# Performance work log

Measured on AMD Instinct MI355X. Metric: run time of the kernel, lower is better.

The kernel has to match this reference:

```python
import jax, jax.numpy as jnp
import numpy as np

N_NODES = 50000
N_EDGES = 1600000
IN_DIM = 128
N_HEADS = 8
OUT_DIM = 16
LEAKY_SLOPE = 0.2


def setup_inputs() -> dict:
    key = jax.random.key(0)
    k1, k2, k3, k4, k5, k6 = jax.random.split(key, 6)
    x = jax.random.normal(k1, (N_NODES, IN_DIM), dtype=jnp.float32)
    W = jax.random.normal(k2, (N_HEADS * OUT_DIM, IN_DIM), dtype=jnp.float32) * (1.414 / np.sqrt(IN_DIM))
    attn_l = jax.random.normal(k3, (N_HEADS, OUT_DIM), dtype=jnp.float32) * 0.5
    attn_r = jax.random.normal(k4, (N_HEADS, OUT_DIM), dtype=jnp.float32) * 0.5
    src = jax.random.randint(k5, (N_EDGES,), 0, N_NODES, dtype=jnp.int64) if jax.config.jax_enable_x64 else jax.random.randint(k5, (N_EDGES,), 0, N_NODES, dtype=jnp.int32)
    dst = jax.random.randint(k6, (N_EDGES,), 0, N_NODES, dtype=src.dtype)
    return {"x": x, "W": W, "attn_l": attn_l, "attn_r": attn_r, "src": src, "dst": dst}


def reference(x, W, attn_l, attn_r, src, dst):
    n = x.shape[0]
    # fc projection -> [N, H, D]
    ft = (x @ W.T).reshape(n, N_HEADS, OUT_DIM)
    # per-node attention logits (bmm with [H,D,1] vector == contraction over D) -> [N, H]
    a1 = jnp.einsum('nhd,hd->nh', ft, attn_l)
    a2 = jnp.einsum('nhd,hd->nh', ft, attn_r)
    # per-edge score: leaky_relu(a1[src] + a2[dst]) -> [E, H]
    e = jax.nn.leaky_relu(a1[src] + a2[dst], negative_slope=LEAKY_SLOPE)
    # segment softmax over incoming edges of each dst node (numerically stable)
    seg_max = jax.ops.segment_max(e, dst, num_segments=n)          # [N, H]
    seg_max = jnp.where(jnp.isfinite(seg_max), seg_max, 0.0)       # isolated nodes -> 0
    e_exp = jnp.exp(e - seg_max[dst])                              # [E, H]
    denom = jax.ops.segment_sum(e_exp, dst, num_segments=n)        # [N, H]
    alpha = e_exp / denom[dst]                                     # [E, H]
    # weighted scatter-sum of src messages -> [N, H, D]
    msgs = ft[src] * alpha[:, :, None]                             # [E, H, D]
    out = jax.ops.segment_sum(msgs, dst, num_segments=n)
    return out
```

## Files before the change

kernel.cpp:

```cpp
#include <hip/hip_runtime.h>
#include <math.h>

#define N_NODES 50000
#define N_EDGES 1600000
#define IN_DIM 128
#define N_HEADS 8
#define OUT_DIM 16
#define HD 128
#define NBUCK 784
#define BCAP 2560
#define CHUNK 4096
#define BIN_BLOCKS ((N_EDGES + CHUNK - 1) / CHUNK)
#define NTILE 3125
#define PBLK ((NTILE + 3) / 4)
#define TROW 132
#define LOG2E 1.4426950408889634f

typedef __attribute__((ext_vector_type(8))) short bf16x8;
typedef __attribute__((ext_vector_type(4))) float f32x4;

__device__ __forceinline__ unsigned short f2bf(float f) {
    union { float f; unsigned int u; } v; v.f = f;
    unsigned int u = v.u;
    unsigned int r = (u + 0x7fffu + ((u >> 16) & 1u)) >> 16;
    return (unsigned short)r;
}

__device__ __forceinline__ void scan_nbuck_excl(int* arr, int* part) {
    int t = threadIdx.x;
    int v0 = 0, v1 = 0, v2 = 0, v3 = 0, cs = 0;
    if (t < NBUCK / 4) {
        v0 = arr[4 * t]; v1 = arr[4 * t + 1]; v2 = arr[4 * t + 2]; v3 = arr[4 * t + 3];
        cs = v0 + v1 + v2 + v3;
    }
    part[t] = cs;
    __syncthreads();
    for (int d = 1; d < 256; d <<= 1) {
        int u = (t >= d) ? part[t - d] : 0;
        __syncthreads();
        part[t] += u;
        __syncthreads();
    }
    if (t < NBUCK / 4) {
        int run = part[t] - cs;
        arr[4 * t] = run; run += v0;
        arr[4 * t + 1] = run; run += v1;
        arr[4 * t + 2] = run; run += v2;
        arr[4 * t + 3] = run;
    }
    __syncthreads();
}

__global__ void k_prep(const float* __restrict__ W, unsigned short* __restrict__ Wb,
                       int* __restrict__ bucket_cnt, int* __restrict__ ovf_cnt) {
    int g = blockIdx.x * 256 + threadIdx.x;
    if (g < NBUCK) bucket_cnt[g] = 0;
    if (g == 0) *ovf_cnt = 0;
    if (g >= (HD * IN_DIM) / 4) return;
    float4 v = ((const float4*)W)[g];
    ushort4 us;
    us.x = f2bf(v.x); us.y = f2bf(v.y); us.z = f2bf(v.z); us.w = f2bf(v.w);
    ((ushort4*)Wb)[g] = us;
}

__global__ __launch_bounds__(256) void k_proj_bin(
    const float* __restrict__ x, const unsigned short* __restrict__ Wb,
    const float* __restrict__ attn_l, const float* __restrict__ attn_r,
    unsigned short* __restrict__ ftb, float* __restrict__ a1, float* __restrict__ a2,
    const int* __restrict__ src, const int* __restrict__ dst,
    unsigned int* __restrict__ region, int* __restrict__ bucket_cnt,
    int* __restrict__ ovf_cnt, unsigned int* __restrict__ ovf) {
    __shared__ __align__(16) char smem[4 * 16 * TROW * 4];
    int tid = threadIdx.x;

    if (blockIdx.x < PBLK) {
        int wid  = tid >> 6;
        int tile = blockIdx.x * 4 + wid;
        if (tile >= NTILE) return;
        int lane = tid & 63;
        int m = lane & 15, q = lane >> 4;
        int node0 = tile * 16;

        const float* xr = x + (size_t)(node0 + m) * IN_DIM + q * 8;
        float4 xa[4][2];
#pragma unroll
        for (int ks = 0; ks < 4; ks++) {
            xa[ks][0] = *(const float4*)(xr + ks * 32);
            xa[ks][1] = *(const float4*)(xr + ks * 32 + 4);
        }
        bf16x8 afr[4];
#pragma unroll
        for (int ks = 0; ks < 4; ks++) {
            afr[ks][0] = (short)f2bf(xa[ks][0].x); afr[ks][1] = (short)f2bf(xa[ks][0].y);
            afr[ks][2] = (short)f2bf(xa[ks][0].z); afr[ks][3] = (short)f2bf(xa[ks][0].w);
            afr[ks][4] = (short)f2bf(xa[ks][1].x); afr[ks][5] = (short)f2bf(xa[ks][1].y);
            afr[ks][6] = (short)f2bf(xa[ks][1].z); afr[ks][7] = (short)f2bf(xa[ks][1].w);
        }

        float* tl = (float*)smem + wid * (16 * TROW);

#pragma unroll
        for (int h = 0; h < N_HEADS; h++) {
            const unsigned short* wrow = Wb + (size_t)(h * 16 + m) * IN_DIM + q * 8;
            f32x4 c = {0.f, 0.f, 0.f, 0.f};
#pragma unroll
            for (int ks = 0; ks < 4; ks++) {
                bf16x8 bfr = *(const bf16x8*)(wrow + ks * 32);
                c = __builtin_amdgcn_mfma_f32_16x16x32_bf16(afr[ks], bfr, c, 0, 0, 0);
            }
#pragma unroll
            for (int r = 0; r < 4; r++)
                tl[(q * 4 + r) * TROW + h * 16 + m] = c[r];
        }

        int nd = lane & 15;
#pragma unroll
        for (int hi = 0; hi < 2; hi++) {
            int hh = (lane >> 4) + hi * 4;
            const float4* rowv = (const float4*)(tl + nd * TROW + hh * 16);
            const float4* alv  = (const float4*)(attn_l + hh * OUT_DIM);
            const float4* arv  = (const float4*)(attn_r + hh * OUT_DIM);
            float sl = 0.f, sr = 0.f;
#pragma unroll
            for (int d4 = 0; d4 < 4; d4++) {
                float4 fv = rowv[d4];
                float4 al = alv[d4];
                float4 ar = arv[d4];
                sl += fv.x * al.x + fv.y * al.y + fv.z * al.z + fv.w * al.w;
                sr += fv.x * ar.x + fv.y * ar.y + fv.z * ar.z + fv.w * ar.w;
            }
            a1[(node0 + nd) * N_HEADS + hh] = sl * LOG2E;
            a2[(node0 + nd) * N_HEADS + hh] = sr * LOG2E;
        }

#pragma unroll
        for (int p = 0; p < 4; p++) {
            int r = p * 4 + q;
            const float* srcp = tl + r * TROW + m * 8;
            float4 f0 = *(const float4*)(srcp);
            float4 f1 = *(const float4*)(srcp + 4);
            ushort4 u0, u1;
            u0.x = f2bf(f0.x); u0.y = f2bf(f0.y); u0.z = f2bf(f0.z); u0.w = f2bf(f0.w);
            u1.x = f2bf(f1.x); u1.y = f2bf(f1.y); u1.z = f2bf(f1.z); u1.w = f2bf(f1.w);
            ushort4* dstp = (ushort4*)(ftb + (size_t)(node0 + r) * HD + m * 8);
            dstp[0] = u0;
            dstp[1] = u1;
        }
    } else {
        unsigned int* stage = (unsigned int*)smem;
        int* hist  = (int*)(smem + 16384);
        int* delta = (int*)(smem + 19520);
        int* part  = (int*)(smem + 22656);

        int t = tid;
        int base = (blockIdx.x - PBLK) * CHUNK;
        int nvalid = min(CHUNK, N_EDGES - base);

        for (int i = t; i < NBUCK; i += 256) hist[i] = 0;
        __syncthreads();

        unsigned int mypack[CHUNK / 256];
#pragma unroll
        for (int k = 0; k < CHUNK / 256; k++) {
            int i = t + k * 256;
            if (i < nvalid) {
                int s = src[base + i];
                int d = dst[base + i];
                unsigned int p = ((unsigned int)d << 16) | (unsigned int)s;
                mypack[k] = p;
                atomicAdd(&hist[d >> 6], 1);
            }
        }
        __syncthreads();
        for (int i = t; i < NBUCK; i += 256) {
            int h = hist[i];
            delta[i] = (h > 0) ? atomicAdd(&bucket_cnt[i], h) : 0;
        }
        __syncthreads();
        scan_nbuck_excl(hist, part);
        for (int i = t; i < NBUCK; i += 256) delta[i] -= hist[i];
        __syncthreads();
#pragma unroll
        for (int k = 0; k < CHUNK / 256; k++) {
            int i = t + k * 256;
            if (i < nvalid) {
                unsigned int p = mypack[k];
                int slot = atomicAdd(&hist[p >> 22], 1);
                stage[slot] = p;
            }
        }
        __syncthreads();
        for (int i = t; i < nvalid; i += 256) {
            unsigned int p = stage[i];
            int b = p >> 22;
            int pos = delta[b] + i;
            if (pos < BCAP) region[(size_t)b * BCAP + pos] = p;
            else { int o = atomicAdd(ovf_cnt, 1); ovf[o] = p; }
        }
    }
}

__global__ __launch_bounds__(256) void k_place(
    const unsigned int* __restrict__ region, const int* __restrict__ bucket_cnt,
    const int* __restrict__ ovf_cnt, const unsigned int* __restrict__ ovf,
    int* __restrict__ offs, unsigned short* __restrict__ esrc) {
    int b = blockIdx.x;
    int t = threadIdx.x;
    __shared__ int sb[NBUCK], part[256];
    __shared__ int hist[64], sc[64], curs[64];
    __shared__ unsigned short sstage[BCAP];

    for (int i = t; i < NBUCK; i += 256) sb[i] = bucket_cnt[i];
    if (t < 64) hist[t] = 0;
    __syncthreads();
    scan_nbuck_excl(sb, part);

    int truec = bucket_cnt[b];
    int base_b = sb[b];
    int rc = min(truec, BCAP);
    bool fits = (truec <= BCAP);
    const unsigned int* reg = region + (size_t)b * BCAP;

    for (int i = t; i < rc; i += 256) atomicAdd(&hist[(reg[i] >> 16) & 63], 1);
    int no = 0;
    if (truec > BCAP) {
        no = *ovf_cnt;
        for (int i = t; i < no; i += 256)
            if ((int)(ovf[i] >> 22) == b) atomicAdd(&hist[(ovf[i] >> 16) & 63], 1);
    }
    __syncthreads();
    int h = (t < 64) ? hist[t] : 0;
    if (t < 64) sc[t] = h;
    __syncthreads();
    for (int d = 1; d < 64; d <<= 1) {
        int u = (t >= d && t < 64) ? sc[t - d] : 0;
        __syncthreads();
        if (t < 64) sc[t] += u;
        __syncthreads();
    }
    if (t < 64) {
        int pos0 = base_b + sc[t] - h;
        int node = b * 64 + t;
        if (node < N_NODES) offs[node] = pos0;
        curs[t] = pos0;
    }
    if (b == 0 && t == 0) offs[N_NODES] = N_EDGES;
    __syncthreads();
    for (int i = t; i < rc; i += 256) {
        unsigned int p = reg[i];
        int pos = atomicAdd(&curs[(p >> 16) & 63], 1);
        if (fits) sstage[pos - base_b] = (unsigned short)(p & 0xffffu);
        else      esrc[pos] = (unsigned short)(p & 0xffffu);
    }
    if (truec > BCAP) {
        for (int i = t; i < no; i += 256) {
            unsigned int p = ovf[i];
            if ((int)(p >> 22) == b) {
                int pos = atomicAdd(&curs[(p >> 16) & 63], 1);
                esrc[pos] = (unsigned short)(p & 0xffffu);
            }
        }
    }
    __syncthreads();
    if (fits) {
        for (int i = t; i < truec; i += 256)
            esrc[base_b + i] = sstage[i];
    }
}

__global__ __launch_bounds__(256) void k_aggregate(
    const unsigned short* __restrict__ ftb, const float* __restrict__ a1,
    const float* __restrict__ a2, const int* __restrict__ offs,
    const unsigned short* __restrict__ esrc, float* __restrict__ out) {
    int wid  = threadIdx.x >> 6;
    int lane = threadIdx.x & 63;
    int node = blockIdx.x * 4 + wid;

    int off = offs[node];
    int deg = offs[node + 1] - off;
    int hl = lane >> 3;
    float a2h = a2[node * N_HEADS + hl];
    int dimoff = lane * 2;

    const unsigned short* ep = esrc + off;
    float accx = 0.f, accy = 0.f, l = 0.f;

    int nfull = deg & ~15;
    for (int base = 0; base < nfull; base += 16) {
        int sv = (int)ep[base + (lane & 15)];
        float a1v[16];
        unsigned int p[16];
#pragma unroll
        for (int k = 0; k < 16; k++) {
            int s = __builtin_amdgcn_readlane(sv, k);
            a1v[k] = *(a1 + (size_t)s * N_HEADS + hl);
            p[k]   = *(const unsigned int*)(ftb + (size_t)s * HD + dimoff);
        }
#pragma unroll
        for (int k = 0; k < 16; k++) {
            float t = a1v[k] + a2h;
            float u = fmaxf(t, 0.2f * t);
            float e;
            asm("v_exp_f32 %0, %1" : "=v"(e) : "v"(u));
            l += e;
            accx = fmaf(e, __uint_as_float(p[k] << 16), accx);
            accy = fmaf(e, __uint_as_float(p[k] & 0xffff0000u), accy);
        }
    }
    if (nfull < deg) {
        int mye = nfull + (lane & 15);
        int sv = (mye < deg) ? (int)ep[mye] : 0;
#pragma unroll
        for (int k = 0; k < 16; k++) {
            if (nfull + k < deg) {
                int s = __builtin_amdgcn_readlane(sv, k);
                float a1v = *(a1 + (size_t)s * N_HEADS + hl);
                unsigned int p = *(const unsigned int*)(ftb + (size_t)s * HD + dimoff);
                float t = a1v + a2h;
                float u = fmaxf(t, 0.2f * t);
                float e;
                asm("v_exp_f32 %0, %1" : "=v"(e) : "v"(u));
                l += e;
                accx = fmaf(e, __uint_as_float(p << 16), accx);
                accy = fmaf(e, __uint_as_float(p & 0xffff0000u), accy);
            }
        }
    }

    float invl = (deg > 0) ? 1.f / l : 0.f;
    float2 o; o.x = accx * invl; o.y = accy * invl;
    *(float2*)(out + (size_t)node * HD + dimoff) = o;
}

extern "C" void kernel_launch(void* const* d_in, const int* in_sizes, int n_in,
                              void* d_out, int out_size, void* d_ws, size_t ws_size,
                              hipStream_t stream) {
    const float* x      = (const float*)d_in[0];
    const float* W      = (const float*)d_in[1];
    const float* attn_l = (const float*)d_in[2];
    const float* attn_r = (const float*)d_in[3];
    const int*   src    = (const int*)d_in[4];
    const int*   dst    = (const int*)d_in[5];
    float* out = (float*)d_out;

    char* ws = (char*)d_ws;
    size_t o = 0;
    auto alloc = [&](size_t bytes) -> char* {
        char* p = ws + o;
        o = (o + bytes + 255) & ~(size_t)255;
        return p;
    };
    unsigned short* ftb  = (unsigned short*)alloc((size_t)N_NODES * HD * 2);
    float* a1            = (float*)alloc((size_t)N_NODES * N_HEADS * 4);
    float* a2            = (float*)alloc((size_t)N_NODES * N_HEADS * 4);
    unsigned short* Wb   = (unsigned short*)alloc((size_t)HD * IN_DIM * 2);
    unsigned int* region = (unsigned int*)alloc((size_t)NBUCK * BCAP * 4);
    int* bucket_cnt      = (int*)alloc((size_t)NBUCK * 4);
    int* ovf_cnt         = (int*)alloc(4);
    unsigned int* ovf    = (unsigned int*)alloc((size_t)N_EDGES * 4);
    int* offs            = (int*)alloc((size_t)(N_NODES + 1) * 4);
    unsigned short* esrc = (unsigned short*)alloc((size_t)N_EDGES * 2);

    (void)in_sizes; (void)n_in; (void)out_size; (void)ws_size;

    k_prep<<<16, 256, 0, stream>>>(W, Wb, bucket_cnt, ovf_cnt);
    k_proj_bin<<<PBLK + BIN_BLOCKS, 256, 0, stream>>>(
        x, Wb, attn_l, attn_r, ftb, a1, a2,
        src, dst, region, bucket_cnt, ovf_cnt, ovf);
    k_place<<<NBUCK, 256, 0, stream>>>(region, bucket_cnt, ovf_cnt, ovf, offs, esrc);
    k_aggregate<<<N_NODES / 4, 256, 0, stream>>>(ftb, a1, a2, offs, esrc, out);
}
```

Baseline: 199.3 us.

## Software-pipeline aggregate gathers in 64-edge batches with sentinel padding node

The aggregation loop now loads 64 source indices at a time and double-buffers 16-edge gather groups, issuing the next group's a1/ft loads before consuming the current one. Partial batches point at a sentinel node whose features are zero and whose a1 is -inf, so no per-edge branch is needed. Offsets are made wave-uniform with readfirstlane, and an occupancy hint is added to launch bounds. The intent is to hide gather latency with more loads in flight, at the cost of more registers and wasted sentinel loads for low-degree nodes.

```diff
diff --git a/kernel.cpp b/kernel.cpp
--- a/kernel.cpp
+++ b/kernel.cpp
@@ -52,10 +52,14 @@
 }
 
 __global__ void k_prep(const float* __restrict__ W, unsigned short* __restrict__ Wb,
-                       int* __restrict__ bucket_cnt, int* __restrict__ ovf_cnt) {
+                       int* __restrict__ bucket_cnt, int* __restrict__ ovf_cnt,
+                       unsigned short* __restrict__ ftb, float* __restrict__ a1) {
     int g = blockIdx.x * 256 + threadIdx.x;
     if (g < NBUCK) bucket_cnt[g] = 0;
     if (g == 0) *ovf_cnt = 0;
+    if (g < 64) ((unsigned int*)(ftb + (size_t)N_NODES * HD))[g] = 0u;
+    if (g >= 64 && g < 64 + N_HEADS)
+        a1[(size_t)N_NODES * N_HEADS + (g - 64)] = __int_as_float(0xff800000);
     if (g >= (HD * IN_DIM) / 4) return;
     float4 v = ((const float4*)W)[g];
     ushort4 us;
@@ -268,7 +272,34 @@
     }
 }
 
-__global__ __launch_bounds__(256) void k_aggregate(
+__device__ __forceinline__ void consume16(const float* a1v, const unsigned int* p,
+                                          float a2h, float& l, float& accx, float& accy) {
+#pragma unroll
+    for (int k = 0; k < 16; k++) {
+        float t = a1v[k] + a2h;
+        float u = fmaxf(t, 0.2f * t);
+        float e;
+        asm("v_exp_f32 %0, %1" : "=v"(e) : "v"(u));
+        l += e;
+        accx = fmaf(e, __uint_as_float(p[k] << 16), accx);
+        accy = fmaf(e, __uint_as_float(p[k] & 0xffff0000u), accy);
+    }
+}
+
+template <int GB>
+__device__ __forceinline__ void issue16(int sv, const float* __restrict__ a1,
+                                        const unsigned short* __restrict__ ftb,
+                                        int hl, int dimoff,
+                                        float* a1v, unsigned int* p) {
+#pragma unroll
+    for (int k = 0; k < 16; k++) {
+        int s = __builtin_amdgcn_readlane(sv, GB + k);
+        a1v[k] = a1[(size_t)s * N_HEADS + hl];
+        p[k]   = *(const unsigned int*)(ftb + (size_t)s * HD + dimoff);
+    }
+}
+
+__global__ __launch_bounds__(256, 4) void k_aggregate(
     const unsigned short* __restrict__ ftb, const float* __restrict__ a1,
     const float* __restrict__ a2, const int* __restrict__ offs,
     const unsigned short* __restrict__ esrc, float* __restrict__ out) {
@@ -276,8 +307,8 @@
     int lane = threadIdx.x & 63;
     int node = blockIdx.x * 4 + wid;
 
-    int off = offs[node];
-    int deg = offs[node + 1] - off;
+    int off = __builtin_amdgcn_readfirstlane(offs[node]);
+    int deg = __builtin_amdgcn_readfirstlane(offs[node + 1]) - off;
     int hl = lane >> 3;
     float a2h = a2[node * N_HEADS + hl];
     int dimoff = lane * 2;
@@ -285,46 +316,24 @@
     const unsigned short* ep = esrc + off;
     float accx = 0.f, accy = 0.f, l = 0.f;
 
-    int nfull = deg & ~15;
-    for (int base = 0; base < nfull; base += 16) {
-        int sv = (int)ep[base + (lane & 15)];
-        float a1v[16];
-        unsigned int p[16];
-#pragma unroll
-        for (int k = 0; k < 16; k++) {
-            int s = __builtin_amdgcn_readlane(sv, k);
-            a1v[k] = *(a1 + (size_t)s * N_HEADS + hl);
-            p[k]   = *(const unsigned int*)(ftb + (size_t)s * HD + dimoff);
-        }
-#pragma unroll
-        for (int k = 0; k < 16; k++) {
-            float t = a1v[k] + a2h;
-            float u = fmaxf(t, 0.2f * t);
-            float e;
-            asm("v_exp_f32 %0, %1" : "=v"(e) : "v"(u));
-            l += e;
-            accx = fmaf(e, __uint_as_float(p[k] << 16), accx);
-            accy = fmaf(e, __uint_as_float(p[k] & 0xffff0000u), accy);
-        }
-    }
-    if (nfull < deg) {
-        int mye = nfull + (lane & 15);
-        int sv = (mye < deg) ? (int)ep[mye] : 0;
-#pragma unroll
-        for (int k = 0; k < 16; k++) {
-            if (nfull + k < deg) {
-                int s = __builtin_amdgcn_readlane(sv, k);
-                float a1v = *(a1 + (size_t)s * N_HEADS + hl);
-                unsigned int p = *(const unsigned int*)(ftb + (size_t)s * HD + dimoff);
-                float t = a1v + a2h;
-                float u = fmaxf(t, 0.2f * t);
-                float e;
-                asm("v_exp_f32 %0, %1" : "=v"(e) : "v"(u));
-                l += e;
-                accx = fmaf(e, __uint_as_float(p << 16), accx);
-                accy = fmaf(e, __uint_as_float(p & 0xffff0000u), accy);
-            }
-        }
+    int done = 0;
+    while (done < deg) {
+        int nb = deg - done;
+        if (nb > 64) nb = 64;
+        int v = (int)ep[done + lane];
+        int sv = (lane < nb) ? v : N_NODES;
+
+        float a1A[16], a1B[16];
+        unsigned int pA[16], pB[16];
+        issue16<0>(sv, a1, ftb, hl, dimoff, a1A, pA);
+        if (nb > 16) issue16<16>(sv, a1, ftb, hl, dimoff, a1B, pB);
+        consume16(a1A, pA, a2h, l, accx, accy);
+        if (nb > 32) issue16<32>(sv, a1, ftb, hl, dimoff, a1A, pA);
+        if (nb > 16) consume16(a1B, pB, a2h, l, accx, accy);
+        if (nb > 48) issue16<48>(sv, a1, ftb, hl, dimoff, a1B, pB);
+        if (nb > 32) consume16(a1A, pA, a2h, l, accx, accy);
+        if (nb > 48) consume16(a1B, pB, a2h, l, accx, accy);
+        done += 64;
     }
 
     float invl = (deg > 0) ? 1.f / l : 0.f;
@@ -350,8 +359,8 @@
         o = (o + bytes + 255) & ~(size_t)255;
         return p;
     };
-    unsigned short* ftb  = (unsigned short*)alloc((size_t)N_NODES * HD * 2);
-    float* a1            = (float*)alloc((size_t)N_NODES * N_HEADS * 4);
+    unsigned short* ftb  = (unsigned short*)alloc((size_t)(N_NODES + 1) * HD * 2);
+    float* a1            = (float*)alloc((size_t)(N_NODES + 1) * N_HEADS * 4);
     float* a2            = (float*)alloc((size_t)N_NODES * N_HEADS * 4);
     unsigned short* Wb   = (unsigned short*)alloc((size_t)HD * IN_DIM * 2);
     unsigned int* region = (unsigned int*)alloc((size_t)NBUCK * BCAP * 4);
@@ -359,11 +368,11 @@
     int* ovf_cnt         = (int*)alloc(4);
     unsigned int* ovf    = (unsigned int*)alloc((size_t)N_EDGES * 4);
     int* offs            = (int*)alloc((size_t)(N_NODES + 1) * 4);
-    unsigned short* esrc = (unsigned short*)alloc((size_t)N_EDGES * 2);
+    unsigned short* esrc = (unsigned short*)alloc((size_t)N_EDGES * 2 + 256);
 
     (void)in_sizes; (void)n_in; (void)out_size; (void)ws_size;
 
-    k_prep<<<16, 256, 0, stream>>>(W, Wb, bucket_cnt, ovf_cnt);
+    k_prep<<<16, 256, 0, stream>>>(W, Wb, bucket_cnt, ovf_cnt, ftb, a1);
     k_proj_bin<<<PBLK + BIN_BLOCKS, 256, 0, stream>>>(
         x, Wb, attn_l, attn_r, ftb, a1, a2,
         src, dst, region, bucket_cnt, ovf_cnt, ovf);
```

New measurement: 195.1 us (median of 2 runs). 2.1% less time.
